# Optimization experiments

Measured on AMD Instinct MI355X. Metric: run time of the kernel, lower is better.

Reference implementation:

```python
import jax, jax.numpy as jnp
import numpy as np
from jax import lax

T, Nn, K, IN, H1, H2, G, P, HEADS = 64, 2048, 32, 256, 128, 128, 256, 60, 3


def setup_inputs() -> dict:
    key = jax.random.key(0)
    ks = jax.random.split(key, 20)
    s = 0.05  # weight scale to keep activations sane
    return {
        'h': jax.random.normal(ks[0], (T, Nn, IN), jnp.float32),
        'neigh': jax.random.randint(ks[1], (Nn, K), 0, Nn),
        'Npop': jnp.ones((1,), jnp.float32) * 1e6,
        'I': jax.random.uniform(ks[2], (T,), jnp.float32) * 1e4,
        'R': jax.random.uniform(ks[3], (T,), jnp.float32) * 1e4,
        'S': jax.random.uniform(ks[4], (T,), jnp.float32) * 9e5,
        'It': jax.random.uniform(ks[5], (T,), jnp.float32),
        'Rt': jax.random.uniform(ks[6], (T,), jnp.float32),
        'fc1': jax.random.normal(ks[7], (HEADS, IN, H1), jnp.float32) * s,
        'fc2': jax.random.normal(ks[8], (HEADS * H1, H2), jnp.float32) * s,
        'gru_Wih': jax.random.normal(ks[9], (3 * G, H2), jnp.float32) * s,
        'gru_Whh': jax.random.normal(ks[10], (3 * G, G), jnp.float32) * s,
        'gru_bih': jax.random.normal(ks[11], (3 * G,), jnp.float32) * s,
        'gru_bhh': jax.random.normal(ks[12], (3 * G,), jnp.float32) * s,
        'res1_W': jax.random.normal(ks[13], (2 * P, G + 2), jnp.float32) * s,
        'res1_b': jax.random.normal(ks[14], (2 * P,), jnp.float32) * s,
        'res2_W': jax.random.normal(ks[15], (2, G + 2), jnp.float32) * s,
        'res2_b': jax.random.normal(ks[16], (2,), jnp.float32) * s,
        'hx0': jax.random.normal(ks[17], (G,), jnp.float32),
    }


def _input_attention(iz, neigh):
    # cosine^4 edge scores, unnormalized weighted sum of neighbor feats
    src = iz[neigh]                                  # [N,K,d]
    dot = jnp.einsum('nkd,nd->nk', src, iz)
    nsrc = jnp.sqrt(jnp.einsum('nkd,nkd->nk', src, src))
    ndst = jnp.sqrt(jnp.sum(iz * iz, axis=-1))[:, None]
    e = (dot / nsrc / ndst) ** 4                     # [N,K]
    return jnp.einsum('nk,nkd->nd', e, src)


def _gat_head(x, W, neigh):
    # dot-product edge attention + per-node softmax + weighted reduce
    z = x @ W                                        # [N,H]
    src = z[neigh]                                   # [N,K,H]
    e = jnp.einsum('nkd,nd->nk', src, z)             # [N,K]
    a = jax.nn.softmax(e, axis=1)
    return jnp.einsum('nk,nkd->nd', a, src)


def _gru_cell(x, hx, Wih, Whh, bih, bhh):
    gi = Wih @ x + bih                               # [3G]
    gh = Whh @ hx + bhh
    ir, iz, inn = jnp.split(gi, 3)
    hr, hz, hn = jnp.split(gh, 3)
    r = jax.nn.sigmoid(ir + hr)
    zg = jax.nn.sigmoid(iz + hz)
    n = jnp.tanh(inn + r * hn)
    return (1.0 - zg) * n + zg * hx


def reference(h, neigh, Npop, I, R, S, It, Rt, fc1, fc2, gru_Wih, gru_Whh,
              gru_bih, gru_bhh, res1_W, res1_b, res2_W, res2_b, hx0):
    Np = Npop[0]

    def step(hx, xs):
        h_t, I_t, R_t, S_t, It_t, Rt_t = xs
        ih = _input_attention(h_t, neigh)                       # [N,in]
        heads = jax.vmap(lambda W: _gat_head(ih, W, neigh))(fc1)  # [3,N,H1]
        c = jax.nn.relu(jnp.transpose(heads, (1, 0, 2)).reshape(Nn, HEADS * H1))
        c = _gat_head(c, fc2, neigh)                            # [N,H2]
        pooled = jnp.max(jax.nn.relu(c), axis=0)                # [H2]
        hx = _gru_cell(pooled, hx, gru_Wih, gru_Whh, gru_bih, gru_bhh)
        nhx = jnp.concatenate([hx, It_t[None], Rt_t[None]])     # [G+2]
        pred = res1_W @ nhx + res1_b                            # [2P]
        ab = res2_W @ nhx + res2_b
        a_s = jax.nn.sigmoid(ab[0])
        b_s = jax.nn.sigmoid(ab[1])
        new_I = pred[0::2]
        new_R = pred[1::2]

        def sir(st, _):
            lI, lR, lS = st
            dI = a_s * lI * (lS / Np) - b_s * lI
            dR = b_s * lI
            nI = lI + lax.stop_gradient(dI)
            nR = lR + lax.stop_gradient(dR)
            nS = Np - nI - nR
            return (nI, nR, nS), (dI, dR)

        _, (pI, pR) = lax.scan(sir, (I_t, R_t, S_t), None, length=P)
        return hx, (new_I, new_R, pI, pR)

    _, (new_I, new_R, phy_I, phy_R) = lax.scan(step, hx0, (h, I, R, S, It, Rt))
    return (new_I, new_R, phy_I.reshape(-1), phy_R.reshape(-1))
```

## Files before the change

kernel.cpp:

```cpp
#include <hip/hip_runtime.h>
#include <hip/hip_bf16.h>
#include <math.h>

#define T_STEPS 64
#define NN      2048
#define KN      32
#define IND     256
#define H1D     128
#define C1D     384
#define H2D     128
#define GD      256
#define PD      60
#define GRU_NB  8

#define BITREV5_INIT {0,16,8,24,4,20,12,28,2,18,10,26,6,22,14,30, \
                      1,17,9,25,5,21,13,29,3,19,11,27,7,23,15,31}

__device__ __forceinline__ float xpose_reduce32(float part[32], int lane) {
#pragma unroll
    for (int i = 0; i < 16; ++i) {
        float send = (lane & 1) ? part[i] : part[i + 16];
        float keep = (lane & 1) ? part[i + 16] : part[i];
        part[i] = keep + __shfl_xor(send, 1);
    }
#pragma unroll
    for (int i = 0; i < 8; ++i) {
        float send = (lane & 2) ? part[i] : part[i + 8];
        float keep = (lane & 2) ? part[i + 8] : part[i];
        part[i] = keep + __shfl_xor(send, 2);
    }
#pragma unroll
    for (int i = 0; i < 4; ++i) {
        float send = (lane & 4) ? part[i] : part[i + 4];
        float keep = (lane & 4) ? part[i + 4] : part[i];
        part[i] = keep + __shfl_xor(send, 4);
    }
#pragma unroll
    for (int i = 0; i < 2; ++i) {
        float send = (lane & 8) ? part[i] : part[i + 2];
        float keep = (lane & 8) ? part[i + 2] : part[i];
        part[i] = keep + __shfl_xor(send, 8);
    }
    {
        float send = (lane & 16) ? part[0] : part[1];
        float keep = (lane & 16) ? part[1] : part[0];
        part[0] = keep + __shfl_xor(send, 16);
    }
    return part[0] + __shfl_xor(part[0], 32);
}

__global__ __launch_bounds__(256) void norms_kernel(const float* __restrict__ h,
                                                    float* __restrict__ norms,
                                                    int t_base) {
    int gw   = (int)((blockIdx.x * blockDim.x + threadIdx.x) >> 6);
    int lane = threadIdx.x & 63;
    int n    = gw & (NN - 1);
    int tloc = gw >> 11;
    const float* row = h + ((size_t)(t_base + tloc) * NN + n) * IND;
    float s = 0.f;
#pragma unroll
    for (int q = 0; q < 4; ++q) { float v = row[lane + 64 * q]; s += v * v; }
#pragma unroll
    for (int off = 32; off > 0; off >>= 1) s += __shfl_xor(s, off);
    if (lane == 0) norms[(size_t)tloc * NN + n] = sqrtf(s);
}

__global__ __launch_bounds__(256) void input_attn_kernel(const float* __restrict__ h,
                                                         const int* __restrict__ neigh,
                                                         const float* __restrict__ norms,
                                                         float* __restrict__ ih,
                                                         int t_base) {
    const int BR[32] = BITREV5_INIT;
    int gw   = (int)((blockIdx.x << 2) | (threadIdx.x >> 6));
    int n    = gw & (NN - 1);
    int tloc = gw >> 11;
    int lane = threadIdx.x & 63;
    const float* hT  = h + (size_t)(t_base + tloc) * NN * IND;
    const float* nrm = norms + (size_t)tloc * NN;

    const float* dst = hT + (size_t)n * IND;
    float d0 = dst[lane], d1 = dst[lane + 64], d2 = dst[lane + 128], d3 = dst[lane + 192];

    int   jreg = neigh[n * KN + (lane & 31)];
    float nj   = nrm[jreg];
    float ndst = nrm[n];

    float part[32];
#pragma unroll
    for (int i = 0; i < 32; ++i) {
        int jk = __shfl(jreg, BR[i]);
        const float* srow = hT + (size_t)jk * IND;
        part[i] = srow[lane] * d0 + srow[lane + 64] * d1
                + srow[lane + 128] * d2 + srow[lane + 192] * d3;
    }
    float dot = xpose_reduce32(part, lane);

    float r  = dot / (nj * ndst);
    float r2 = r * r;
    float e  = r2 * r2;

    float a0 = 0.f, a1 = 0.f, a2 = 0.f, a3 = 0.f;
#pragma unroll
    for (int kk = 0; kk < KN; ++kk) {
        float ek = __shfl(e, kk);
        int   jk = __shfl(jreg, kk);
        const float* srow = hT + (size_t)jk * IND;
        a0 += ek * srow[lane];
        a1 += ek * srow[lane + 64];
        a2 += ek * srow[lane + 128];
        a3 += ek * srow[lane + 192];
    }
    float* orow = ih + (size_t)gw * IND;
    orow[lane]       = a0;
    orow[lane + 64]  = a1;
    orow[lane + 128] = a2;
    orow[lane + 192] = a3;
}

__global__ __launch_bounds__(256) void matmul_f32(const float* __restrict__ A,
                                                  const float* __restrict__ B,
                                                  float* __restrict__ C,
                                                  int M, int N, int K) {
    __shared__ float As[16][65];
    __shared__ float Bs[16][68];
    int tid  = threadIdx.x;
    int row0 = blockIdx.y * 64;
    int col0 = blockIdx.x * 64;
    int tr = tid >> 4, tc = tid & 15;
    float acc[4][4] = {};
    int la_m = tid >> 2;
    int la_k = (tid & 3) * 4;
    int lb_k = tid >> 4;
    int lb_n = (tid & 15) * 4;
    for (int k0 = 0; k0 < K; k0 += 16) {
        float4 av = *(const float4*)(A + (size_t)(row0 + la_m) * K + k0 + la_k);
        float4 bv = *(const float4*)(B + (size_t)(k0 + lb_k) * N + col0 + lb_n);
        __syncthreads();
        As[la_k + 0][la_m] = av.x; As[la_k + 1][la_m] = av.y;
        As[la_k + 2][la_m] = av.z; As[la_k + 3][la_m] = av.w;
        *(float4*)&Bs[lb_k][lb_n] = bv;
        __syncthreads();
#pragma unroll
        for (int kk = 0; kk < 16; ++kk) {
            float a[4], b[4];
#pragma unroll
            for (int r = 0; r < 4; ++r) a[r] = As[kk][tr * 4 + r];
#pragma unroll
            for (int c = 0; c < 4; ++c) b[c] = Bs[kk][tc * 4 + c];
#pragma unroll
            for (int r = 0; r < 4; ++r)
#pragma unroll
                for (int c = 0; c < 4; ++c) acc[r][c] += a[r] * b[c];
        }
    }
#pragma unroll
    for (int r = 0; r < 4; ++r) {
        float4 v = { acc[r][0], acc[r][1], acc[r][2], acc[r][3] };
        *(float4*)(C + (size_t)(row0 + tr * 4 + r) * N + col0 + tc * 4) = v;
    }
}

__global__ __launch_bounds__(192) void gat_heads_kernel(const float* __restrict__ z1,
                                                        const int* __restrict__ neigh,
                                                        float* __restrict__ c) {
    const int BR[32] = BITREV5_INIT;
    int n    = blockIdx.x & (NN - 1);
    const float* ztbl = z1 + (size_t)(blockIdx.x >> 11) * NN * C1D;
    int head = threadIdx.x >> 6;
    int lane = threadIdx.x & 63;

    const float* dst = ztbl + (size_t)n * C1D + head * H1D;
    float d0 = dst[lane], d1 = dst[lane + 64];
    int jreg = neigh[n * KN + (lane & 31)];

    float part[32];
#pragma unroll
    for (int i = 0; i < 32; ++i) {
        int jk = __shfl(jreg, BR[i]);
        const float* srow = ztbl + (size_t)jk * C1D + head * H1D;
        part[i] = srow[lane] * d0 + srow[lane + 64] * d1;
    }
    float dot = xpose_reduce32(part, lane);

    float m = dot;
#pragma unroll
    for (int off = 16; off > 0; off >>= 1) m = fmaxf(m, __shfl_xor(m, off));
    float p = __expf(dot - m);
    float s = p;
#pragma unroll
    for (int off = 16; off > 0; off >>= 1) s += __shfl_xor(s, off);
    p /= s;

    float a0 = 0.f, a1 = 0.f;
#pragma unroll
    for (int kk = 0; kk < KN; ++kk) {
        float pk = __shfl(p, kk);
        int   jk = __shfl(jreg, kk);
        const float* srow = ztbl + (size_t)jk * C1D + head * H1D;
        a0 += pk * srow[lane];
        a1 += pk * srow[lane + 64];
    }
    size_t base = (size_t)blockIdx.x * C1D + (size_t)head * H1D;
    c[base + lane]      = fmaxf(a0, 0.f);
    c[base + lane + 64] = fmaxf(a1, 0.f);
}

__global__ __launch_bounds__(256) void gat_final_kernel(const float* __restrict__ z2,
                                                        const int* __restrict__ neigh,
                                                        float* __restrict__ c2) {
    const int BR[32] = BITREV5_INIT;
    int gw   = (int)((blockIdx.x << 2) | (threadIdx.x >> 6));
    int n    = gw & (NN - 1);
    const float* ztbl = z2 + (size_t)(gw >> 11) * NN * H2D;
    int lane = threadIdx.x & 63;

    const float* dst = ztbl + (size_t)n * H2D;
    float d0 = dst[lane], d1 = dst[lane + 64];
    int jreg = neigh[n * KN + (lane & 31)];

    float part[32];
#pragma unroll
    for (int i = 0; i < 32; ++i) {
        int jk = __shfl(jreg, BR[i]);
        const float* srow = ztbl + (size_t)jk * H2D;
        part[i] = srow[lane] * d0 + srow[lane + 64] * d1;
    }
    float dot = xpose_reduce32(part, lane);

    float m = dot;
#pragma unroll
    for (int off = 16; off > 0; off >>= 1) m = fmaxf(m, __shfl_xor(m, off));
    float p = __expf(dot - m);
    float s = p;
#pragma unroll
    for (int off = 16; off > 0; off >>= 1) s += __shfl_xor(s, off);
    p /= s;

    float a0 = 0.f, a1 = 0.f;
#pragma unroll
    for (int kk = 0; kk < KN; ++kk) {
        float pk = __shfl(p, kk);
        int   jk = __shfl(jreg, kk);
        const float* srow = ztbl + (size_t)jk * H2D;
        a0 += pk * srow[lane];
        a1 += pk * srow[lane + 64];
    }
    c2[(size_t)gw * H2D + lane]      = fmaxf(a0, 0.f);
    c2[(size_t)gw * H2D + lane + 64] = fmaxf(a1, 0.f);
}

__global__ __launch_bounds__(128) void pool_part_kernel(const float* __restrict__ c2,
                                                        float* __restrict__ ppart) {
    int j = threadIdx.x;
    int tloc  = blockIdx.x >> 4;
    int slice = blockIdx.x & 15;
    const float* base = c2 + ((size_t)tloc * NN + slice * 128) * H2D;
    float mx = 0.f;
    for (int q = 0; q < 128; ++q) mx = fmaxf(mx, base[(size_t)q * H2D + j]);
    ppart[(size_t)blockIdx.x * H2D + j] = mx;
}
__global__ __launch_bounds__(128) void pool_reduce_kernel(const float* __restrict__ ppart,
                                                          float* __restrict__ pooled,
                                                          int t_base) {
    int j = threadIdx.x;
    const float* base = ppart + (size_t)blockIdx.x * 16 * H2D;
    float mx = 0.f;
#pragma unroll
    for (int q = 0; q < 16; ++q) mx = fmaxf(mx, base[(size_t)q * H2D + j]);
    pooled[(t_base + blockIdx.x) * H2D + j] = mx;
}

__global__ void prep_W1(const float* __restrict__ fc1, float* __restrict__ W1,
                        unsigned int* __restrict__ cnt) {
    int i = blockIdx.x * 256 + threadIdx.x;
    if (i < 256 * 384) {
        int d = i / 384, cf = i % 384;
        int hd = cf >> 7, j = cf & 127;
        W1[i] = fc1[(size_t)hd * 256 * 128 + (size_t)d * 128 + j];
    }
    if (i < T_STEPS) cnt[i] = 0u;
}

__global__ __launch_bounds__(256) void gi_all_kernel(const float* __restrict__ Wih,
                                                     const float* __restrict__ bih,
                                                     const float* __restrict__ pooled,
                                                     float* __restrict__ gi_all) {
    __shared__ float p_s[H2D];
    int t  = blockIdx.x / 3;
    int ob = (blockIdx.x % 3) * 256;
    if (threadIdx.x < H2D) p_s[threadIdx.x] = pooled[t * H2D + threadIdx.x];
    __syncthreads();
    int o = ob + threadIdx.x;
    float acc = bih[o];
    const float* wr = Wih + (size_t)o * H2D;
#pragma unroll 4
    for (int d = 0; d < H2D; ++d) acc += wr[d] * p_s[d];
    gi_all[t * 768 + o] = acc;
}

__global__ __launch_bounds__(768) void gru_reg_kernel(const float* __restrict__ Whh,
                                                      const float* __restrict__ bhh,
                                                      const float* __restrict__ gi_all,
                                                      const float* __restrict__ hx0,
                                                      float* hx_all,
                                                      unsigned int* cnt) {
    __shared__ float4 hx_pad[72];
    __shared__ __align__(16) float hx_lin[GD];
    __shared__ float gh_s[96];
    int b   = blockIdx.x;
    int tid = threadIdx.x;
    int row_local = tid >> 3;
    int sub       = tid & 7;
    int chunk     = row_local >> 5;
    int r_in      = row_local & 31;
    int grow      = chunk * GD + b * 32 + r_in;

    float4 wreg[8];
    const float4* wrow = (const float4*)(Whh + (size_t)grow * GD + sub * 32);
#pragma unroll
    for (int i = 0; i < 8; ++i) wreg[i] = wrow[i];
    float bias = (sub == 0) ? bhh[grow] : 0.f;

    for (int t = 0; t < T_STEPS; ++t) {
        if (t > 0) {
            if (tid == 0) {
                while (__hip_atomic_load(&cnt[t - 1], __ATOMIC_ACQUIRE,
                                         __HIP_MEMORY_SCOPE_AGENT) < GRU_NB)
                    __builtin_amdgcn_s_sleep(1);
            }
            __syncthreads();
        }
        const float* hsrc = (t == 0) ? hx0 : (hx_all + (size_t)(t - 1) * GD);
        if (tid < 64) {
            float4 v;
            v.x = __hip_atomic_load(hsrc + tid * 4 + 0, __ATOMIC_RELAXED, __HIP_MEMORY_SCOPE_AGENT);
            v.y = __hip_atomic_load(hsrc + tid * 4 + 1, __ATOMIC_RELAXED, __HIP_MEMORY_SCOPE_AGENT);
            v.z = __hip_atomic_load(hsrc + tid * 4 + 2, __ATOMIC_RELAXED, __HIP_MEMORY_SCOPE_AGENT);
            v.w = __hip_atomic_load(hsrc + tid * 4 + 3, __ATOMIC_RELAXED, __HIP_MEMORY_SCOPE_AGENT);
            hx_pad[(tid >> 3) * 9 + (tid & 7)] = v;
            ((float4*)hx_lin)[tid] = v;
        }
        __syncthreads();

        float acc = 0.f;
#pragma unroll
        for (int i = 0; i < 8; ++i) {
            float4 hv = hx_pad[sub * 9 + i];
            float4 wv = wreg[i];
            acc += wv.x * hv.x + wv.y * hv.y + wv.z * hv.z + wv.w * hv.w;
        }
        acc += __shfl_xor(acc, 1);
        acc += __shfl_xor(acc, 2);
        acc += __shfl_xor(acc, 4);
        if (sub == 0) gh_s[row_local] = acc + bias;
        __syncthreads();

        if (tid < 32) {
            int u = b * 32 + tid;
            float gi_r = gi_all[t * 768 + u];
            float gi_z = gi_all[t * 768 + 256 + u];
            float gi_n = gi_all[t * 768 + 512 + u];
            float r  = 1.f / (1.f + expf(-(gi_r + gh_s[tid])));
            float zg = 1.f / (1.f + expf(-(gi_z + gh_s[32 + tid])));
            float nn = tanhf(gi_n + r * gh_s[64 + tid]);
            float hnew = (1.f - zg) * nn + zg * hx_lin[u];
            __hip_atomic_store(&hx_all[(size_t)t * GD + u], hnew,
                               __ATOMIC_RELAXED, __HIP_MEMORY_SCOPE_AGENT);
            __threadfence();
        }
        __syncthreads();
        if (tid == 0)
            __hip_atomic_fetch_add(&cnt[t], 1u, __ATOMIC_RELEASE,
                                   __HIP_MEMORY_SCOPE_AGENT);
    }
}

__global__ __launch_bounds__(128) void res_sir_kernel(const float* __restrict__ hx_all,
                                                      const float* __restrict__ It,
                                                      const float* __restrict__ Rt,
                                                      const float* __restrict__ r1W,
                                                      const float* __restrict__ r1b,
                                                      const float* __restrict__ r2W,
                                                      const float* __restrict__ r2b,
                                                      const float* __restrict__ I,
                                                      const float* __restrict__ R,
                                                      const float* __restrict__ S,
                                                      const float* __restrict__ Npop,
                                                      float* __restrict__ out) {
    __shared__ float nhx[258];
    __shared__ float ab_s[2];
    int t = blockIdx.x, tid = threadIdx.x;
    for (int i = tid; i < GD; i += 128) nhx[i] = hx_all[t * GD + i];
    if (tid == 0) { nhx[256] = It[t]; nhx[257] = Rt[t]; }
    __syncthreads();
    if (tid < 120) {
        float acc = r1b[tid];
        const float* wr = r1W + tid * 258;
        for (int d = 0; d < 258; ++d) acc += wr[d] * nhx[d];
        int idx = t * 60 + (tid >> 1);
        if (tid & 1) out[3840 + idx] = acc;
        else         out[idx] = acc;
    }
    if (tid == 120 || tid == 121) {
        int q = tid - 120;
        float acc = r2b[q];
        const float* wr = r2W + q * 258;
        for (int d = 0; d < 258; ++d) acc += wr[d] * nhx[d];
        ab_s[q] = acc;
    }
    __syncthreads();
    if (tid == 0) {
        float a_s = 1.f / (1.f + expf(-ab_s[0]));
        float b_s = 1.f / (1.f + expf(-ab_s[1]));
        float Np = Npop[0];
        float lI = I[t], lR = R[t], lS = S[t];
        for (int p = 0; p < PD; ++p) {
            float dI = a_s * lI * (lS / Np) - b_s * lI;
            float dR = b_s * lI;
            lI += dI;
            lR += dR;
            lS = Np - lI - lR;
            out[7680  + t * 60 + p] = dI;
            out[11520 + t * 60 + p] = dR;
        }
    }
}

extern "C" void kernel_launch(void* const* d_in, const int* in_sizes, int n_in,
                              void* d_out, int out_size, void* d_ws, size_t ws_size,
                              hipStream_t stream) {
    const float* h    = (const float*)d_in[0];
    const int*   ng   = (const int*)  d_in[1];
    const float* Npop = (const float*)d_in[2];
    const float* I_   = (const float*)d_in[3];
    const float* R_   = (const float*)d_in[4];
    const float* S_   = (const float*)d_in[5];
    const float* It   = (const float*)d_in[6];
    const float* Rt   = (const float*)d_in[7];
    const float* fc1  = (const float*)d_in[8];
    const float* fc2  = (const float*)d_in[9];
    const float* gWih = (const float*)d_in[10];
    const float* gWhh = (const float*)d_in[11];
    const float* gbih = (const float*)d_in[12];
    const float* gbhh = (const float*)d_in[13];
    const float* r1W  = (const float*)d_in[14];
    const float* r1b  = (const float*)d_in[15];
    const float* r2W  = (const float*)d_in[16];
    const float* r2b  = (const float*)d_in[17];
    const float* hx0  = (const float*)d_in[18];
    float* out = (float*)d_out;

    char* w = (char*)d_ws;
    float* pooled = (float*)w; w += (size_t)T_STEPS * H2D * 4;
    float* hx_all = (float*)w; w += (size_t)T_STEPS * GD * 4;
    float* W1     = (float*)w; w += (size_t)256 * 384 * 4;
    float* gi_all = (float*)w; w += (size_t)T_STEPS * 768 * 4;
    float* ppart  = (float*)w; w += (size_t)T_STEPS * 16 * H2D * 4;
    unsigned int* cnt = (unsigned int*)w; w += 256;
    size_t fixed = (size_t)(w - (char*)d_ws);

    int Tc = 64;
    while (Tc > 1) {
        size_t need = fixed + (size_t)Tc * (8192 + 2ull * 2048 * 384 * 4);
        if (need <= ws_size) break;
        Tc >>= 1;
    }
    float* norms = (float*)w; w += (size_t)Tc * NN * 4;
    float* bufA  = (float*)w; w += (size_t)Tc * NN * C1D * 4;
    float* bufB  = (float*)w;

    prep_W1<<<(256 * 384 + 255) / 256, 256, 0, stream>>>(fc1, W1, cnt);

    for (int t0 = 0; t0 < T_STEPS; t0 += Tc) {
        int M = Tc * NN;
        norms_kernel      <<<Tc * NN / 4, 256, 0, stream>>>(h, norms, t0);
        input_attn_kernel <<<Tc * NN / 4, 256, 0, stream>>>(h, ng, norms, bufA, t0);
        matmul_f32<<<dim3(384 / 64, M / 64), 256, 0, stream>>>(bufA, W1, bufB, M, 384, 256);
        gat_heads_kernel  <<<Tc * NN, 192, 0, stream>>>(bufB, ng, bufA);
        matmul_f32<<<dim3(128 / 64, M / 64), 256, 0, stream>>>(bufA, fc2, bufB, M, 128, 384);
        gat_final_kernel  <<<Tc * NN / 4, 256, 0, stream>>>(bufB, ng, bufA);
        pool_part_kernel  <<<Tc * 16, 128, 0, stream>>>(bufA, ppart);
        pool_reduce_kernel<<<Tc, 128, 0, stream>>>(ppart, pooled, t0);
    }

    gi_all_kernel<<<T_STEPS * 3, 256, 0, stream>>>(gWih, gbih, pooled, gi_all);
    gru_reg_kernel<<<GRU_NB, 768, 0, stream>>>(gWhh, gbhh, gi_all, hx0, hx_all, cnt);
    res_sir_kernel<<<T_STEPS, 128, 0, stream>>>(hx_all, It, Rt, r1W, r1b, r2W, r2b,
                                                I_, R_, S_, Npop, out);
}
```

Baseline: 1.682 ms.

## Keep gathered neighbor rows in registers and split input attention across two waves

The three attention kernels now hold the gathered neighbor feature rows in registers (r0/r1) from the score pass and reuse them in the weighted-sum pass, instead of gathering every neighbor row from global memory a second time. The first transpose-reduce stage is folded into the load loop. The input attention kernel also splits each node's 256-wide feature across two waves, combining the partial dot products through shared memory with a block barrier. This halves its register footprint, and the grid is doubled to match. The register caching adds 64 live floats per thread, which can lower occupancy, and the barrier couples the two waves of each node.

```diff
diff --git a/kernel.cpp b/kernel.cpp
--- a/kernel.cpp
+++ b/kernel.cpp
@@ -16,13 +16,7 @@
 #define BITREV5_INIT {0,16,8,24,4,20,12,28,2,18,10,26,6,22,14,30, \
                       1,17,9,25,5,21,13,29,3,19,11,27,7,23,15,31}
 
-__device__ __forceinline__ float xpose_reduce32(float part[32], int lane) {
-#pragma unroll
-    for (int i = 0; i < 16; ++i) {
-        float send = (lane & 1) ? part[i] : part[i + 16];
-        float keep = (lane & 1) ? part[i + 16] : part[i];
-        part[i] = keep + __shfl_xor(send, 1);
-    }
+__device__ __forceinline__ float xpose_reduce16(float part[16], int lane) {
 #pragma unroll
     for (int i = 0; i < 8; ++i) {
         float send = (lane & 2) ? part[i] : part[i + 8];
@@ -71,50 +65,58 @@
                                                          float* __restrict__ ih,
                                                          int t_base) {
     const int BR[32] = BITREV5_INIT;
-    int gw   = (int)((blockIdx.x << 2) | (threadIdx.x >> 6));
+    __shared__ float hd_s[2][2][32];
+    int wave    = threadIdx.x >> 6;
+    int nodeloc = wave >> 1;
+    int half    = wave & 1;
+    int lane    = threadIdx.x & 63;
+    int gw   = (int)((blockIdx.x << 1) | nodeloc);
     int n    = gw & (NN - 1);
     int tloc = gw >> 11;
-    int lane = threadIdx.x & 63;
     const float* hT  = h + (size_t)(t_base + tloc) * NN * IND;
     const float* nrm = norms + (size_t)tloc * NN;
 
-    const float* dst = hT + (size_t)n * IND;
-    float d0 = dst[lane], d1 = dst[lane + 64], d2 = dst[lane + 128], d3 = dst[lane + 192];
+    const float* dst = hT + (size_t)n * IND + half * 128;
+    float d0 = dst[lane], d1 = dst[lane + 64];
 
     int   jreg = neigh[n * KN + (lane & 31)];
     float nj   = nrm[jreg];
     float ndst = nrm[n];
 
-    float part[32];
-#pragma unroll
-    for (int i = 0; i < 32; ++i) {
-        int jk = __shfl(jreg, BR[i]);
-        const float* srow = hT + (size_t)jk * IND;
-        part[i] = srow[lane] * d0 + srow[lane + 64] * d1
-                + srow[lane + 128] * d2 + srow[lane + 192] * d3;
-    }
-    float dot = xpose_reduce32(part, lane);
+    float r0[32], r1[32], comb[16];
+#pragma unroll
+    for (int i = 0; i < 16; ++i) {
+        int ja = __shfl(jreg, BR[i]);
+        int jb = __shfl(jreg, BR[i + 16]);
+        const float* sa = hT + (size_t)ja * IND + half * 128;
+        const float* sb = hT + (size_t)jb * IND + half * 128;
+        r0[i]      = sa[lane]; r1[i]      = sa[lane + 64];
+        r0[i + 16] = sb[lane]; r1[i + 16] = sb[lane + 64];
+        float pa = r0[i] * d0 + r1[i] * d1;
+        float pb = r0[i + 16] * d0 + r1[i + 16] * d1;
+        float send = (lane & 1) ? pa : pb;
+        float keep = (lane & 1) ? pb : pa;
+        comb[i] = keep + __shfl_xor(send, 1);
+    }
+    float hdot = xpose_reduce16(comb, lane);
+    if (lane < 32) hd_s[nodeloc][half][lane] = hdot;
+    __syncthreads();
+    float dot = hdot + hd_s[nodeloc][half ^ 1][lane & 31];
 
     float r  = dot / (nj * ndst);
     float r2 = r * r;
     float e  = r2 * r2;
 
-    float a0 = 0.f, a1 = 0.f, a2 = 0.f, a3 = 0.f;
-#pragma unroll
-    for (int kk = 0; kk < KN; ++kk) {
-        float ek = __shfl(e, kk);
-        int   jk = __shfl(jreg, kk);
-        const float* srow = hT + (size_t)jk * IND;
-        a0 += ek * srow[lane];
-        a1 += ek * srow[lane + 64];
-        a2 += ek * srow[lane + 128];
-        a3 += ek * srow[lane + 192];
-    }
-    float* orow = ih + (size_t)gw * IND;
-    orow[lane]       = a0;
-    orow[lane + 64]  = a1;
-    orow[lane + 128] = a2;
-    orow[lane + 192] = a3;
+    float a0 = 0.f, a1 = 0.f;
+#pragma unroll
+    for (int i = 0; i < 32; ++i) {
+        float ek = __shfl(e, BR[i]);
+        a0 += ek * r0[i];
+        a1 += ek * r1[i];
+    }
+    float* orow = ih + (size_t)gw * IND + half * 128;
+    orow[lane]      = a0;
+    orow[lane + 64] = a1;
 }
 
 __global__ __launch_bounds__(256) void matmul_f32(const float* __restrict__ A,
@@ -173,14 +175,22 @@
     float d0 = dst[lane], d1 = dst[lane + 64];
     int jreg = neigh[n * KN + (lane & 31)];
 
-    float part[32];
-#pragma unroll
-    for (int i = 0; i < 32; ++i) {
-        int jk = __shfl(jreg, BR[i]);
-        const float* srow = ztbl + (size_t)jk * C1D + head * H1D;
-        part[i] = srow[lane] * d0 + srow[lane + 64] * d1;
-    }
-    float dot = xpose_reduce32(part, lane);
+    float r0[32], r1[32], comb[16];
+#pragma unroll
+    for (int i = 0; i < 16; ++i) {
+        int ja = __shfl(jreg, BR[i]);
+        int jb = __shfl(jreg, BR[i + 16]);
+        const float* sa = ztbl + (size_t)ja * C1D + head * H1D;
+        const float* sb = ztbl + (size_t)jb * C1D + head * H1D;
+        r0[i]      = sa[lane]; r1[i]      = sa[lane + 64];
+        r0[i + 16] = sb[lane]; r1[i + 16] = sb[lane + 64];
+        float pa = r0[i] * d0 + r1[i] * d1;
+        float pb = r0[i + 16] * d0 + r1[i + 16] * d1;
+        float send = (lane & 1) ? pa : pb;
+        float keep = (lane & 1) ? pb : pa;
+        comb[i] = keep + __shfl_xor(send, 1);
+    }
+    float dot = xpose_reduce16(comb, lane);
 
     float m = dot;
 #pragma unroll
@@ -193,12 +203,10 @@
 
     float a0 = 0.f, a1 = 0.f;
 #pragma unroll
-    for (int kk = 0; kk < KN; ++kk) {
-        float pk = __shfl(p, kk);
-        int   jk = __shfl(jreg, kk);
-        const float* srow = ztbl + (size_t)jk * C1D + head * H1D;
-        a0 += pk * srow[lane];
-        a1 += pk * srow[lane + 64];
+    for (int i = 0; i < 32; ++i) {
+        float pk = __shfl(p, BR[i]);
+        a0 += pk * r0[i];
+        a1 += pk * r1[i];
     }
     size_t base = (size_t)blockIdx.x * C1D + (size_t)head * H1D;
     c[base + lane]      = fmaxf(a0, 0.f);
@@ -218,14 +226,22 @@
     float d0 = dst[lane], d1 = dst[lane + 64];
     int jreg = neigh[n * KN + (lane & 31)];
 
-    float part[32];
-#pragma unroll
-    for (int i = 0; i < 32; ++i) {
-        int jk = __shfl(jreg, BR[i]);
-        const float* srow = ztbl + (size_t)jk * H2D;
-        part[i] = srow[lane] * d0 + srow[lane + 64] * d1;
-    }
-    float dot = xpose_reduce32(part, lane);
+    float r0[32], r1[32], comb[16];
+#pragma unroll
+    for (int i = 0; i < 16; ++i) {
+        int ja = __shfl(jreg, BR[i]);
+        int jb = __shfl(jreg, BR[i + 16]);
+        const float* sa = ztbl + (size_t)ja * H2D;
+        const float* sb = ztbl + (size_t)jb * H2D;
+        r0[i]      = sa[lane]; r1[i]      = sa[lane + 64];
+        r0[i + 16] = sb[lane]; r1[i + 16] = sb[lane + 64];
+        float pa = r0[i] * d0 + r1[i] * d1;
+        float pb = r0[i + 16] * d0 + r1[i + 16] * d1;
+        float send = (lane & 1) ? pa : pb;
+        float keep = (lane & 1) ? pb : pa;
+        comb[i] = keep + __shfl_xor(send, 1);
+    }
+    float dot = xpose_reduce16(comb, lane);
 
     float m = dot;
 #pragma unroll
@@ -238,12 +254,10 @@
 
     float a0 = 0.f, a1 = 0.f;
 #pragma unroll
-    for (int kk = 0; kk < KN; ++kk) {
-        float pk = __shfl(p, kk);
-        int   jk = __shfl(jreg, kk);
-        const float* srow = ztbl + (size_t)jk * H2D;
-        a0 += pk * srow[lane];
-        a1 += pk * srow[lane + 64];
+    for (int i = 0; i < 32; ++i) {
+        float pk = __shfl(p, BR[i]);
+        a0 += pk * r0[i];
+        a1 += pk * r1[i];
     }
     c2[(size_t)gw * H2D + lane]      = fmaxf(a0, 0.f);
     c2[(size_t)gw * H2D + lane + 64] = fmaxf(a1, 0.f);
@@ -474,7 +488,7 @@
     for (int t0 = 0; t0 < T_STEPS; t0 += Tc) {
         int M = Tc * NN;
         norms_kernel      <<<Tc * NN / 4, 256, 0, stream>>>(h, norms, t0);
-        input_attn_kernel <<<Tc * NN / 4, 256, 0, stream>>>(h, ng, norms, bufA, t0);
+        input_attn_kernel <<<Tc * NN / 2, 256, 0, stream>>>(h, ng, norms, bufA, t0);
         matmul_f32<<<dim3(384 / 64, M / 64), 256, 0, stream>>>(bufA, W1, bufB, M, 384, 256);
         gat_heads_kernel  <<<Tc * NN, 192, 0, stream>>>(bufB, ng, bufA);
         matmul_f32<<<dim3(128 / 64, M / 64), 256, 0, stream>>>(bufA, fc2, bufB, M, 128, 384);
```

After: 1.719 ms. 2.2% more time.
